# Kernel optimization log

Measured on AMD Instinct MI355X. Metric: run time of the kernel, lower is better.

Reference implementation:

```python
import jax, jax.numpy as jnp
import numpy as np

S, HID, H, D, G = 2048, 4096, 32, 128, 2   # seq, hidden, heads, head_dim, kv groups
ROT = D // 2                               # rotary applied to first half of head_dim
QKV = HID + 2 * G * D                      # 4608


def setup_inputs() -> dict:
    key = jax.random.key(0)
    k1, k2, k3 = jax.random.split(key, 3)
    sc = 0.02
    return {
        "hidden_states": jax.random.normal(k1, (S, HID), jnp.float32),
        "W_qkv": jax.random.normal(k2, (HID, QKV), jnp.float32) * sc,
        "b_qkv": jnp.zeros((QKV,), jnp.float32),
        "W_dense": jax.random.normal(k3, (HID, HID), jnp.float32) * sc,
    }


def _rope(x, pos):
    # x: [S, n_heads, ROT]; interleaved-pair rotation (ChatGLM2 convention)
    half = ROT // 2
    inv_freq = 10000.0 ** (-jnp.arange(0, ROT, 2, dtype=jnp.float32) / ROT)  # [half]
    theta = pos[:, None] * inv_freq                                          # [S, half]
    cos = jnp.cos(theta)[:, None, :]
    sin = jnp.sin(theta)[:, None, :]
    xp = x.reshape(x.shape[0], x.shape[1], half, 2)
    x0, x1 = xp[..., 0], xp[..., 1]
    out = jnp.stack([x0 * cos - x1 * sin, x1 * cos + x0 * sin], axis=-1)
    return out.reshape(x.shape)


def reference(hidden_states, W_qkv, b_qkv, W_dense):
    qkv = hidden_states @ W_qkv + b_qkv            # [S, QKV]
    q = qkv[:, : H * D].reshape(S, H, D)           # [S, H, D]
    k = qkv[:, H * D : H * D + G * D].reshape(S, G, D)
    v = qkv[:, H * D + G * D :].reshape(S, G, D)

    pos = jnp.arange(S, dtype=jnp.float32)
    q = jnp.concatenate([_rope(q[..., :ROT], pos), q[..., ROT:]], axis=-1)
    k = jnp.concatenate([_rope(k[..., :ROT], pos), k[..., ROT:]], axis=-1)

    gidx = jnp.arange(H) % G                       # head -> kv group (MQA/GQA)
    kh = k[:, gidx, :]                             # [S, H, D]
    vh = v[:, gidx, :]

    scores = jnp.einsum('shd,thd->hst', q, kh) / jnp.sqrt(jnp.float32(D))
    causal = jnp.tril(jnp.ones((S, S), bool))
    scores = jnp.where(causal[None], scores, jnp.float32(-1e9))
    p = jax.nn.softmax(scores, axis=-1)            # [H, S, S]
    ctx = jnp.einsum('hst,thd->shd', p, vh).reshape(S, HID)
    return ctx @ W_dense
```

## Files before the change

kernel.cpp:

```cpp
#include <hip/hip_runtime.h>
#include <hip/hip_bf16.h>

#define S_LEN 2048
#define HIDN  4096
#define NH    32
#define HD    128
#define QKV_N 4608
#define K_OFF 4096
#define V_OFF 4352
#define SCALE 0.08838834764831845f
#define MOFF  8.0f

typedef __attribute__((ext_vector_type(8))) short   short8;
typedef __attribute__((ext_vector_type(4))) float   f32x4;
typedef __attribute__((ext_vector_type(4))) unsigned short ushort4v;
typedef __attribute__((ext_vector_type(8))) unsigned short ushort8;

typedef __attribute__((address_space(1))) const unsigned int GU32;
typedef __attribute__((address_space(3))) unsigned int LU32;

__device__ __forceinline__ void async16(const void* g, void* l) {
  __builtin_amdgcn_global_load_lds((GU32*)g, (LU32*)l, 16, 0, 0);
}

__device__ __forceinline__ unsigned short f2bf(float x) {
  __hip_bfloat16 h = __float2bfloat16(x);
  return *reinterpret_cast<unsigned short*>(&h);
}
__device__ __forceinline__ float bf2f(unsigned short u) {
  __hip_bfloat16 h = *reinterpret_cast<__hip_bfloat16*>(&u);
  return __bfloat162float(h);
}

__global__ void k_cvt_bf16(const float* __restrict__ in, unsigned short* __restrict__ out, int n4) {
  int i = blockIdx.x * 256 + threadIdx.x;
  if (i >= n4) return;
  const float4 v = reinterpret_cast<const float4*>(in)[i];
  ushort4v o = { f2bf(v.x), f2bf(v.y), f2bf(v.z), f2bf(v.w) };
  reinterpret_cast<ushort4v*>(out)[i] = o;
}

__global__ __launch_bounds__(256) void k_transpose_cvt(const float* __restrict__ W,
                                                       unsigned short* __restrict__ WT,
                                                       int K, int N) {
  __shared__ float tl[64][65];
  const int n0 = blockIdx.x * 64, k0 = blockIdx.y * 64;
  const int t = threadIdx.x;
  const int r = t >> 4, c4 = (t & 15) << 2;
#pragma unroll
  for (int p = 0; p < 4; ++p) {
    int krow = p * 16 + r;
    const float4 v = *reinterpret_cast<const float4*>(&W[(size_t)(k0 + krow) * N + n0 + c4]);
    tl[krow][c4 + 0] = v.x; tl[krow][c4 + 1] = v.y;
    tl[krow][c4 + 2] = v.z; tl[krow][c4 + 3] = v.w;
  }
  __syncthreads();
#pragma unroll
  for (int p = 0; p < 4; ++p) {
    int nrow = p * 16 + r;
    ushort4v o = { f2bf(tl[c4 + 0][nrow]), f2bf(tl[c4 + 1][nrow]),
                   f2bf(tl[c4 + 2][nrow]), f2bf(tl[c4 + 3][nrow]) };
    *reinterpret_cast<ushort4v*>(&WT[(size_t)(n0 + nrow) * K + k0 + c4]) = o;
  }
}

template <int BIAS, int OUTBF>
__global__ __launch_bounds__(256, 2) void k_gemm_bt(const unsigned short* __restrict__ A,
                                                    const unsigned short* __restrict__ Bt,
                                                    const float* __restrict__ bias,
                                                    void* __restrict__ Cout,
                                                    int M, int N, int K) {
  __shared__ __align__(16) unsigned char lds[32768];
  const int tid = threadIdx.x;
  const int l = tid & 63, w = tid >> 6;
  const int wr = w >> 1, wc = w & 1;
  const int l16 = l & 15, lh = l >> 4;
  const int nx = N >> 7;
  const int cpx = gridDim.x >> 3;
  const int wg = (blockIdx.x & 7) * cpx + (blockIdx.x >> 3);
  const int m0 = (wg / nx) * 128, n0 = (wg % nx) * 128;
  const size_t rowK = (size_t)K * 2;
  const char* Ab = (const char*)A + (size_t)m0 * rowK;
  const char* Bb = (const char*)Bt + (size_t)n0 * rowK;
  f32x4 acc[4][4] = {};
  const int nkt = K >> 6;
  for (int kt = 0; kt < nkt; ++kt) {
    const int kbyte = kt << 7;
#pragma unroll
    for (int rr = 0; rr < 4; ++rr) {
      int off = rr * 4096 + tid * 16;
      int row = off >> 7;
      int col = (off & 127) ^ ((row & 7) << 4);
      async16(Ab + (size_t)row * rowK + kbyte + col, lds + off);
    }
#pragma unroll
    for (int rr = 0; rr < 4; ++rr) {
      int off = rr * 4096 + tid * 16;
      int row = off >> 7;
      int col = (off & 127) ^ ((row & 7) << 4);
      async16(Bb + (size_t)row * rowK + kbyte + col, lds + 16384 + off);
    }
    __syncthreads();
#pragma unroll
    for (int kk = 0; kk < 2; ++kk) {
      short8 af[4], bfr[4];
#pragma unroll
      for (int m = 0; m < 4; ++m) {
        int arow = wr * 64 + m * 16 + l16;
        int byte = (arow << 7) + kk * 64 + lh * 16;
        byte ^= (arow & 7) << 4;
        af[m] = *reinterpret_cast<const short8*>(lds + byte);
      }
#pragma unroll
      for (int n = 0; n < 4; ++n) {
        int brow = wc * 64 + n * 16 + l16;
        int byte = (brow << 7) + kk * 64 + lh * 16;
        byte ^= (brow & 7) << 4;
        bfr[n] = *reinterpret_cast<const short8*>(lds + 16384 + byte);
      }
#pragma unroll
      for (int m = 0; m < 4; ++m)
#pragma unroll
        for (int n = 0; n < 4; ++n)
          acc[m][n] = __builtin_amdgcn_mfma_f32_16x16x32_bf16(af[m], bfr[n], acc[m][n], 0, 0, 0);
    }
    __syncthreads();
  }
#pragma unroll
  for (int m = 0; m < 4; ++m) {
    int grow = m0 + wr * 64 + m * 16 + lh * 4;
#pragma unroll
    for (int n = 0; n < 4; ++n) {
      int gcol = n0 + wc * 64 + n * 16 + l16;
      float bv = BIAS ? bias[gcol] : 0.f;
      f32x4 v = acc[m][n];
#pragma unroll
      for (int j = 0; j < 4; ++j) {
        float val = v[j] + bv;
        if (OUTBF) ((unsigned short*)Cout)[(size_t)(grow + j) * N + gcol] = f2bf(val);
        else       ((float*)Cout)[(size_t)(grow + j) * N + gcol] = val;
      }
    }
  }
}

__global__ void k_rope(unsigned short* __restrict__ qkv) {
  const int p = blockIdx.x * 64 + threadIdx.x;
  const int s = blockIdx.y;
  const int i = p & 31;
  const int hh = p >> 5;
  const int col = (hh < 32) ? (hh * HD + 2 * i) : (K_OFF + (hh - 32) * HD + 2 * i);
  unsigned int* ptr = (unsigned int*)(qkv + (size_t)s * QKV_N + col);
  unsigned int both = *ptr;
  float x0 = bf2f((unsigned short)(both & 0xffffu));
  float x1 = bf2f((unsigned short)(both >> 16));
  float inv = expf(-0.28782313662425572f * (float)i);
  float theta = (float)s * inv;
  float sn, cs;
  sincosf(theta, &sn, &cs);
  float y0 = x0 * cs - x1 * sn;
  float y1 = x1 * cs + x0 * sn;
  *ptr = (unsigned int)f2bf(y0) | ((unsigned int)f2bf(y1) << 16);
}

__global__ __launch_bounds__(256) void k_transpose_v(const unsigned short* __restrict__ qkv,
                                                     unsigned short* __restrict__ Vt) {
  __shared__ __align__(16) unsigned short tl[64][72];
  const int st = blockIdx.x * 64;
  const int dt = blockIdx.y * 64;
  const int g = blockIdx.z;
  const int t = threadIdx.x;
  const int r = t >> 3;
  const int seg = (t & 7) * 8;
#pragma unroll
  for (int p = 0; p < 2; ++p) {
    int srow = p * 32 + r;
    ushort8 v = *reinterpret_cast<const ushort8*>(
        &qkv[(size_t)(st + srow) * QKV_N + V_OFF + g * HD + dt + seg]);
    *reinterpret_cast<ushort8*>(&tl[srow][seg]) = v;
  }
  __syncthreads();
#pragma unroll
  for (int p = 0; p < 2; ++p) {
    int drow = p * 32 + r;
    ushort8 o;
#pragma unroll
    for (int i = 0; i < 8; ++i) o[i] = tl[seg + i][drow];
    *reinterpret_cast<ushort8*>(&Vt[((size_t)g * HD + dt + drow) * S_LEN + st + seg]) = o;
  }
}

__device__ __forceinline__ void stage_kv(const char* Kb, const char* Vb,
                                         unsigned char* ldsK, unsigned char* ldsV, int tid) {
  __builtin_amdgcn_sched_barrier(0);
#pragma unroll
  for (int rr = 0; rr < 4; ++rr) {
    int off = rr * 4096 + tid * 16;
    int row = off >> 8;
    int col = (off & 255) ^ ((row & 15) << 4);
    async16(Kb + (size_t)row * (QKV_N * 2) + col, ldsK + off);
  }
#pragma unroll
  for (int rr = 0; rr < 4; ++rr) {
    int off = rr * 4096 + tid * 16;
    int row = off >> 7;
    int col = (off & 127) ^ ((row & 7) << 4);
    async16(Vb + (size_t)row * (S_LEN * 2) + col, ldsV + off);
  }
  __builtin_amdgcn_sched_barrier(0);
}

__global__ __launch_bounds__(256) void k_attn(const unsigned short* __restrict__ qkv,
                                              const unsigned short* __restrict__ Vt,
                                              unsigned short* __restrict__ ctx) {
  __shared__ __align__(16) unsigned char lds[73728];
  const int tid = threadIdx.x;
  const int l = tid & 63, w = tid >> 6;
  const int l16 = l & 15, lh = l >> 4;
  const int h = blockIdx.y;
  const int g = h & 1;
  const int b = blockIdx.x;
  const int tA = 31 - b;
  const int nA = tA + 1;
  const int nT = nA + b + 1;
  const int q0A = tA * 64, q0B = b * 64;

  const char* Kbase = (const char*)(qkv + K_OFF + g * HD);
  const char* Vbase = (const char*)(Vt + ((size_t)g * HD) * S_LEN);

  short8 vones;
#pragma unroll
  for (int e = 0; e < 8; ++e) vones[e] = (short)0x3F80;

  short8 qf[4];
#pragma unroll
  for (int ks = 0; ks < 4; ++ks)
    qf[ks] = *reinterpret_cast<const short8*>(
        qkv + (size_t)(q0A + w * 16 + l16) * QKV_N + h * HD + ks * 32 + lh * 8);

  f32x4 o[8] = {};
  f32x4 lacc = {};

  stage_kv(Kbase, Vbase, lds, lds + 32768, tid);

  for (int it = 0; it < nT; ++it) {
    const int phase = (it >= nA) ? 1 : 0;
    const int kt = phase ? (it - nA) : it;
    const int q0 = phase ? q0B : q0A;
    const int k0 = kt << 6;
    const int nxt = it + 1;
    if (nxt < nT) {
      const int kn = ((nxt >= nA) ? (nxt - nA) : nxt) << 6;
      stage_kv(Kbase + (size_t)kn * (QKV_N * 2), Vbase + (size_t)kn * 2,
               lds + (nxt & 1) * 16384, lds + 32768 + (nxt & 1) * 16384, tid);
      asm volatile("s_waitcnt vmcnt(8)" ::: "memory");
    } else {
      asm volatile("s_waitcnt vmcnt(0)" ::: "memory");
    }
    __builtin_amdgcn_s_barrier();
    __builtin_amdgcn_sched_barrier(0);

    const unsigned char* Kl = lds + (it & 1) * 16384;
    const unsigned char* Vl = lds + 32768 + (it & 1) * 16384;

    f32x4 sf[4] = {};
    __builtin_amdgcn_s_setprio(1);
#pragma unroll
    for (int n = 0; n < 4; ++n) {
      int krow = n * 16 + l16;
      int swz = (krow & 15) << 4;
#pragma unroll
      for (int ks = 0; ks < 4; ++ks) {
        int byte = (krow << 8) + ks * 64 + lh * 16;
        short8 kf = *reinterpret_cast<const short8*>(Kl + (byte ^ swz));
        sf[n] = __builtin_amdgcn_mfma_f32_16x16x32_bf16(qf[ks], kf, sf[n], 0, 0, 0);
      }
    }
    __builtin_amdgcn_s_setprio(0);

    const int qrow0 = q0 + w * 16 + lh * 4;
    unsigned char* Pb = lds + 65536 + w * 2048;
#pragma unroll
    for (int n = 0; n < 4; ++n) {
      int key = k0 + n * 16 + l16;
#pragma unroll
      for (int j = 0; j < 4; ++j) {
        float v = sf[n][j] * SCALE - MOFF;
        v = (key <= qrow0 + j) ? v : -1e30f;
        int row = lh * 4 + j;
        int byte = (row << 7) + (n * 16 + l16) * 2;
        byte ^= (row & 7) << 4;
        *(unsigned short*)(Pb + byte) = f2bf(__expf(v));
      }
    }

    __builtin_amdgcn_s_setprio(1);
#pragma unroll
    for (int kk = 0; kk < 2; ++kk) {
      int pbyte = (l16 << 7) + kk * 64 + lh * 16;
      pbyte ^= (l16 & 7) << 4;
      short8 pa = *reinterpret_cast<const short8*>(Pb + pbyte);
      lacc = __builtin_amdgcn_mfma_f32_16x16x32_bf16(pa, vones, lacc, 0, 0, 0);
#pragma unroll
      for (int n8 = 0; n8 < 8; ++n8) {
        int vrow = n8 * 16 + l16;
        int vbyte = (vrow << 7) + kk * 64 + lh * 16;
        vbyte ^= (vrow & 7) << 4;
        short8 vb = *reinterpret_cast<const short8*>(Vl + vbyte);
        o[n8] = __builtin_amdgcn_mfma_f32_16x16x32_bf16(pa, vb, o[n8], 0, 0, 0);
      }
    }
    __builtin_amdgcn_s_setprio(0);

    if (it == nA - 1) {
#pragma unroll
      for (int n8 = 0; n8 < 8; ++n8) {
        int col = h * HD + n8 * 16 + l16;
#pragma unroll
        for (int j = 0; j < 4; ++j) {
          int row = q0A + w * 16 + lh * 4 + j;
          ctx[(size_t)row * HIDN + col] = f2bf(o[n8][j] / lacc[j]);
        }
      }
#pragma unroll
      for (int n8 = 0; n8 < 8; ++n8) o[n8] = f32x4{0.f, 0.f, 0.f, 0.f};
      lacc = f32x4{0.f, 0.f, 0.f, 0.f};
      __builtin_amdgcn_sched_barrier(0);
#pragma unroll
      for (int ks = 0; ks < 4; ++ks)
        qf[ks] = *reinterpret_cast<const short8*>(
            qkv + (size_t)(q0B + w * 16 + l16) * QKV_N + h * HD + ks * 32 + lh * 8);
      __builtin_amdgcn_sched_barrier(0);
    }
    __builtin_amdgcn_s_barrier();
  }

#pragma unroll
  for (int n8 = 0; n8 < 8; ++n8) {
    int col = h * HD + n8 * 16 + l16;
#pragma unroll
    for (int j = 0; j < 4; ++j) {
      int row = q0B + w * 16 + lh * 4 + j;
      ctx[(size_t)row * HIDN + col] = f2bf(o[n8][j] / lacc[j]);
    }
  }
}

extern "C" void kernel_launch(void* const* d_in, const int* in_sizes, int n_in,
                              void* d_out, int out_size, void* d_ws, size_t ws_size,
                              hipStream_t stream) {
  const float* hidden = (const float*)d_in[0];
  const float* Wqkv = (const float*)d_in[1];
  const float* bqkv = (const float*)d_in[2];
  const float* Wd = (const float*)d_in[3];
  char* ws = (char*)d_ws;
  unsigned short* hid_bf = (unsigned short*)(ws);
  unsigned short* WqkvT  = (unsigned short*)(ws + 16777216);
  unsigned short* WdT    = (unsigned short*)(ws + 54525952);
  unsigned short* qkv    = (unsigned short*)(ws + 88080384);
  unsigned short* Vt     = (unsigned short*)(ws + 106954752);
  unsigned short* ctx    = (unsigned short*)(ws + 108003328);

  k_cvt_bf16<<<8192, 256, 0, stream>>>(hidden, hid_bf, 2097152);
  k_transpose_cvt<<<dim3(72, 64), 256, 0, stream>>>(Wqkv, WqkvT, 4096, 4608);
  k_transpose_cvt<<<dim3(64, 64), 256, 0, stream>>>(Wd, WdT, 4096, 4096);
  k_gemm_bt<1, 1><<<576, 256, 0, stream>>>(hid_bf, WqkvT, bqkv, qkv, 2048, 4608, 4096);
  k_rope<<<dim3(17, 2048), 64, 0, stream>>>(qkv);
  k_transpose_v<<<dim3(32, 2, 2), 256, 0, stream>>>(qkv, Vt);
  k_attn<<<dim3(16, 32), 256, 0, stream>>>(qkv, Vt, ctx);
  k_gemm_bt<0, 0><<<512, 256, 0, stream>>>(ctx, WdT, nullptr, d_out, 2048, 4096, 4096);
}
```

Baseline: 297.3 us.

## Double-buffer GEMM LDS loads and precompute RoPE sin/cos table

The bf16 MFMA GEMM now keeps two LDS buffers (64KB) and issues the async global-to-LDS loads for the next K tile before computing the current one. It waits with explicit vmcnt counts and raw s_barrier instead of a full __syncthreads, so memory latency can overlap with MFMA work. Separately, RoPE cos/sin values are computed once into a workspace table by a new small kernel rather than recomputed with expf/sincosf per element. The larger LDS footprint may lower occupancy below the 2-blocks launch bound, and the hand-written waitcnt logic must match the number of outstanding loads exactly.

After: 327.1 us. 1.1x slower.

```diff
diff --git a/kernel.cpp b/kernel.cpp
--- a/kernel.cpp
+++ b/kernel.cpp
@@ -70,7 +70,7 @@
                                                     const float* __restrict__ bias,
                                                     void* __restrict__ Cout,
                                                     int M, int N, int K) {
-  __shared__ __align__(16) unsigned char lds[32768];
+  __shared__ __align__(16) unsigned char lds[65536];
   const int tid = threadIdx.x;
   const int l = tid & 63, w = tid >> 6;
   const int wr = w >> 1, wc = w & 1;
@@ -84,23 +84,38 @@
   const char* Bb = (const char*)Bt + (size_t)n0 * rowK;
   f32x4 acc[4][4] = {};
   const int nkt = K >> 6;
-  for (int kt = 0; kt < nkt; ++kt) {
-    const int kbyte = kt << 7;
+
+  auto stage = [&](int kbyte, int bsel) {
+    __builtin_amdgcn_sched_barrier(0);
 #pragma unroll
     for (int rr = 0; rr < 4; ++rr) {
       int off = rr * 4096 + tid * 16;
       int row = off >> 7;
       int col = (off & 127) ^ ((row & 7) << 4);
-      async16(Ab + (size_t)row * rowK + kbyte + col, lds + off);
+      async16(Ab + (size_t)row * rowK + kbyte + col, lds + bsel * 16384 + off);
     }
 #pragma unroll
     for (int rr = 0; rr < 4; ++rr) {
       int off = rr * 4096 + tid * 16;
       int row = off >> 7;
       int col = (off & 127) ^ ((row & 7) << 4);
-      async16(Bb + (size_t)row * rowK + kbyte + col, lds + 16384 + off);
-    }
-    __syncthreads();
+      async16(Bb + (size_t)row * rowK + kbyte + col, lds + 32768 + bsel * 16384 + off);
+    }
+    __builtin_amdgcn_sched_barrier(0);
+  };
+
+  stage(0, 0);
+  for (int kt = 0; kt < nkt; ++kt) {
+    if (kt + 1 < nkt) {
+      stage((kt + 1) << 7, (kt + 1) & 1);
+      asm volatile("s_waitcnt vmcnt(8)" ::: "memory");
+    } else {
+      asm volatile("s_waitcnt vmcnt(0)" ::: "memory");
+    }
+    __builtin_amdgcn_s_barrier();
+    __builtin_amdgcn_sched_barrier(0);
+    const unsigned char* Al = lds + (kt & 1) * 16384;
+    const unsigned char* Bl = lds + 32768 + (kt & 1) * 16384;
 #pragma unroll
     for (int kk = 0; kk < 2; ++kk) {
       short8 af[4], bfr[4];
@@ -109,14 +124,14 @@
         int arow = wr * 64 + m * 16 + l16;
         int byte = (arow << 7) + kk * 64 + lh * 16;
         byte ^= (arow & 7) << 4;
-        af[m] = *reinterpret_cast<const short8*>(lds + byte);
+        af[m] = *reinterpret_cast<const short8*>(Al + byte);
       }
 #pragma unroll
       for (int n = 0; n < 4; ++n) {
         int brow = wc * 64 + n * 16 + l16;
         int byte = (brow << 7) + kk * 64 + lh * 16;
         byte ^= (brow & 7) << 4;
-        bfr[n] = *reinterpret_cast<const short8*>(lds + 16384 + byte);
+        bfr[n] = *reinterpret_cast<const short8*>(Bl + byte);
       }
 #pragma unroll
       for (int m = 0; m < 4; ++m)
@@ -124,7 +139,7 @@
         for (int n = 0; n < 4; ++n)
           acc[m][n] = __builtin_amdgcn_mfma_f32_16x16x32_bf16(af[m], bfr[n], acc[m][n], 0, 0, 0);
     }
-    __syncthreads();
+    __builtin_amdgcn_s_barrier();
   }
 #pragma unroll
   for (int m = 0; m < 4; ++m) {
@@ -144,7 +159,17 @@
   }
 }
 
-__global__ void k_rope(unsigned short* __restrict__ qkv) {
+__global__ void k_rope_tab(float* __restrict__ tab) {
+  int idx = blockIdx.x * 256 + threadIdx.x;
+  float inv = expf(-0.28782313662425572f * (float)(idx & 31));
+  float theta = (float)(idx >> 5) * inv;
+  float sn, cs;
+  sincosf(theta, &sn, &cs);
+  tab[idx * 2 + 0] = cs;
+  tab[idx * 2 + 1] = sn;
+}
+
+__global__ void k_rope(unsigned short* __restrict__ qkv, const float* __restrict__ tab) {
   const int p = blockIdx.x * 64 + threadIdx.x;
   const int s = blockIdx.y;
   const int i = p & 31;
@@ -154,12 +179,9 @@
   unsigned int both = *ptr;
   float x0 = bf2f((unsigned short)(both & 0xffffu));
   float x1 = bf2f((unsigned short)(both >> 16));
-  float inv = expf(-0.28782313662425572f * (float)i);
-  float theta = (float)s * inv;
-  float sn, cs;
-  sincosf(theta, &sn, &cs);
-  float y0 = x0 * cs - x1 * sn;
-  float y1 = x1 * cs + x0 * sn;
+  const float2 cssn = reinterpret_cast<const float2*>(tab)[s * 32 + i];
+  float y0 = x0 * cssn.x - x1 * cssn.y;
+  float y1 = x1 * cssn.x + x0 * cssn.y;
   *ptr = (unsigned int)f2bf(y0) | ((unsigned int)f2bf(y1) << 16);
 }
 
@@ -360,12 +382,14 @@
   unsigned short* qkv    = (unsigned short*)(ws + 88080384);
   unsigned short* Vt     = (unsigned short*)(ws + 106954752);
   unsigned short* ctx    = (unsigned short*)(ws + 108003328);
-
+  float*          rtab   = (float*)(ws + 124780544);
+
+  k_rope_tab<<<256, 256, 0, stream>>>(rtab);
   k_cvt_bf16<<<8192, 256, 0, stream>>>(hidden, hid_bf, 2097152);
   k_transpose_cvt<<<dim3(72, 64), 256, 0, stream>>>(Wqkv, WqkvT, 4096, 4608);
   k_transpose_cvt<<<dim3(64, 64), 256, 0, stream>>>(Wd, WdT, 4096, 4096);
   k_gemm_bt<1, 1><<<576, 256, 0, stream>>>(hid_bf, WqkvT, bqkv, qkv, 2048, 4608, 4096);
-  k_rope<<<dim3(17, 2048), 64, 0, stream>>>(qkv);
+  k_rope<<<dim3(17, 2048), 64, 0, stream>>>(qkv, rtab);
   k_transpose_v<<<dim3(32, 2, 2), 256, 0, stream>>>(qkv, Vt);
   k_attn<<<dim3(16, 32), 256, 0, stream>>>(qkv, Vt, ctx);
   k_gemm_bt<0, 0><<<512, 256, 0, stream>>>(ctx, WdT, nullptr, d_out, 2048, 4096, 4096);
```
